# Kernel optimization log

Hardware: AMD Instinct MI355X
Metric: run time of the kernel (lower is better)

The kernel has to match this reference:

```python
import jax, jax.numpy as jnp
import numpy as np

N = 100_000          # num nodes
E = 1_600_000        # undirected edges (mean_degree = 2E/N = 32)
Q = 8                # num_groups
NUM_ITER = 5         # fixed BP iterations (max_num_iter)


def setup_inputs() -> dict:
    key = jax.random.key(0)
    k1, k2, k3, k4 = jax.random.split(key, 4)
    u = jax.random.randint(k1, (E,), 0, N, dtype=jnp.int32)
    v = jax.random.randint(k2, (E,), 0, N, dtype=jnp.int32)
    # directed messages: both orientations of every undirected edge
    src = jnp.concatenate([u, v])                 # [2E] message source i of i->j
    dst = jnp.concatenate([v, u])                 # [2E] message target j of i->j
    # rev[e] = index of the reverse message j->i for edge e = i->j
    rev = jnp.concatenate([jnp.arange(E, 2 * E, dtype=jnp.int32),
                           jnp.arange(E, dtype=jnp.int32)])
    psi0 = jax.random.uniform(k3, (N, Q), dtype=jnp.float32)
    msg0 = jax.random.uniform(k4, (2 * E, Q), dtype=jnp.float32)
    c = 2.0 * E / N  # mean degree
    beta = jnp.asarray(np.log(Q / np.sqrt(c - 1.0) + 1.0), dtype=jnp.float32)
    return dict(beta=beta, psi0=psi0, msg0=msg0, src=src, dst=dst, rev=rev,
                num_iter=NUM_ITER)


def reference(beta, psi0, msg0, src, dst, rev, num_iter):
    N_, Q_ = psi0.shape
    M = msg0.shape[0]
    mean_w = M / (N_ * N_)  # adjacency_matrix.mean() = 2E / N^2 (unweighted)
    psi = psi0 / psi0.sum(1, keepdims=True)   # normalized marginals [N,Q]
    msg = msg0 / msg0.sum(1, keepdims=True)   # normalized messages  [M,Q]
    h = (-beta * mean_w * psi).sum(0)         # external field        [Q]

    def step(carry, _):
        msg, psi, h = carry
        c = jnp.expm1(beta)                          # e^beta - 1
        # per-incoming-edge factor, in log space (scatter_mul -> segment_sum of logs)
        log_f = jnp.log1p(msg * c)                   # [M,Q]
        S = jax.ops.segment_sum(log_f, dst, num_segments=N_)  # [N,Q] prod over k->i
        # message i->j: exclude contribution of reverse edge j->i (cavity)
        logits = h + S[src] - log_f[rev]             # [M,Q]
        new_msg = jax.nn.softmax(logits, axis=-1)    # normalized per message
        diff = jnp.max(jnp.abs(new_msg - msg))
        # marginals from updated messages
        log_f2 = jnp.log1p(new_msg * c)
        S2 = jax.ops.segment_sum(log_f2, dst, num_segments=N_)
        new_psi = jax.nn.softmax(h + S2, axis=-1)    # [N,Q]
        new_h = (-beta * mean_w * new_psi).sum(0)    # [Q]
        return (new_msg, new_psi, new_h), diff

    (msg, psi, h), diffs = jax.lax.scan(step, (msg, psi, h), None, length=int(num_iter))
    return msg, psi, diffs[-1]
```

## Files before the change

### kernel.cpp

```cpp
#include <hip/hip_runtime.h>
#include <math.h>

#define Q 8
#define NUM_ITER 5
#define BLOCK 256
#define EBLK 1024
#define BLOCKA 512
#define NBN 1024
#define NBSHIFT 10
#define MAXBKT 128
#define W 4
#define QS 262144.0f
#define GRED 512

__device__ __forceinline__ void load8(const float* __restrict__ p, float v[Q]) {
    float4 a = ((const float4*)p)[0];
    float4 b = ((const float4*)p)[1];
    v[0]=a.x; v[1]=a.y; v[2]=a.z; v[3]=a.w;
    v[4]=b.x; v[5]=b.y; v[6]=b.z; v[7]=b.w;
}

__device__ __forceinline__ void store8(float* __restrict__ p, const float v[Q]) {
    ((float4*)p)[0] = make_float4(v[0],v[1],v[2],v[3]);
    ((float4*)p)[1] = make_float4(v[4],v[5],v[6],v[7]);
}

__device__ __forceinline__ void softmax8_fast(float l[Q]) {
    float mx = l[0];
    #pragma unroll
    for (int q=1;q<Q;q++) mx = fmaxf(mx, l[q]);
    float s = 0.f;
    #pragma unroll
    for (int q=0;q<Q;q++) { l[q] = __expf(l[q]-mx); s += l[q]; }
    float inv = 1.0f/s;
    #pragma unroll
    for (int q=0;q<Q;q++) l[q] *= inv;
}

__device__ __forceinline__ void pack18(const float lf[Q], int loc, uint4& a, unsigned& x) {
    unsigned v[Q];
    #pragma unroll
    for (int q=0;q<Q;q++) v[q] = (unsigned)__float2int_rn(lf[q]*QS);
    a.x = (v[0]&0xFFFFu) | ((v[1]&0xFFFFu)<<16);
    a.y = (v[2]&0xFFFFu) | ((v[3]&0xFFFFu)<<16);
    a.z = (v[4]&0xFFFFu) | ((v[5]&0xFFFFu)<<16);
    a.w = (v[6]&0xFFFFu) | ((v[7]&0xFFFFu)<<16);
    x = (v[0]>>16) | ((v[1]>>16)<<2) | ((v[2]>>16)<<4) | ((v[3]>>16)<<6)
      | ((v[4]>>16)<<8) | ((v[5]>>16)<<10) | ((v[6]>>16)<<12) | ((v[7]>>16)<<14)
      | ((unsigned)loc<<16);
}

__global__ void k_count(const int* __restrict__ src, const int* __restrict__ dst,
                        int* __restrict__ bcnt, int E, int nbkt) {
    __shared__ int c[4][MAXBKT];
    int wv = threadIdx.x >> 6;
    for (int t=threadIdx.x; t<4*MAXBKT; t+=BLOCK) ((int*)c)[t]=0;
    __syncthreads();
    for (int k = blockIdx.x*BLOCK + threadIdx.x; k < E; k += gridDim.x*BLOCK) {
        atomicAdd(&c[wv][dst[k]>>NBSHIFT], 1);
        atomicAdd(&c[wv][src[k]>>NBSHIFT], 1);
    }
    __syncthreads();
    for (int t=threadIdx.x; t<nbkt; t+=BLOCK) {
        int s = c[0][t]+c[1][t]+c[2][t]+c[3][t];
        if (s) atomicAdd(&bcnt[t], s);
    }
}

__global__ void k_scan(const int* __restrict__ bcnt, int* __restrict__ bucket_start,
                       int* __restrict__ cursor_g, int nbkt) {
    if (threadIdx.x==0 && blockIdx.x==0) {
        int run = 0;
        for (int b=0;b<nbkt;b++) { bucket_start[b]=run; cursor_g[b*16]=run; run += bcnt[b]; }
        bucket_start[nbkt] = run;
    }
}

__global__ void k_psi_init(const float* __restrict__ psi0,
                           const float* __restrict__ beta_p,
                           float mean_w, double* __restrict__ h0, int N) {
    int i = blockIdx.x*BLOCK + threadIdx.x;
    float c[Q];
    #pragma unroll
    for (int q=0;q<Q;q++) c[q]=0.f;
    if (i < N) {
        float p[Q]; load8(psi0 + (size_t)i*Q, p);
        float s = 0.f;
        #pragma unroll
        for (int q=0;q<Q;q++) s += p[q];
        float scale = -beta_p[0]*mean_w/s;
        #pragma unroll
        for (int q=0;q<Q;q++) c[q] = p[q]*scale;
    }
    __shared__ double sm[BLOCK/64][Q];
    #pragma unroll
    for (int q=0;q<Q;q++) {
        double x = (double)c[q];
        #pragma unroll
        for (int off=32;off;off>>=1) x += __shfl_down(x,off);
        if ((threadIdx.x&63)==0) sm[threadIdx.x>>6][q]=x;
    }
    __syncthreads();
    if (threadIdx.x < Q) {
        double x = sm[0][threadIdx.x]+sm[1][threadIdx.x]+sm[2][threadIdx.x]+sm[3][threadIdx.x];
        atomicAdd(h0+threadIdx.x, x);
    }
}

__global__ __launch_bounds__(EBLK) void k_init(const float* __restrict__ msg0,
                       const int* __restrict__ src, const int* __restrict__ dst,
                       const float* __restrict__ beta_p,
                       float* __restrict__ msg,
                       uint4* __restrict__ ebuf_q, unsigned* __restrict__ ebuf_x,
                       int* __restrict__ cursor_g, int E, int nbkt) {
    __shared__ int cnt[MAXBKT], excl[MAXBKT], base[MAXBKT];
    __shared__ int totsh;
    __shared__ uint4 staged[2*EBLK];
    __shared__ unsigned staged_x[2*EBLK];
    __shared__ int gpos[2*EBLK];
    int tid = threadIdx.x;
    for (int t=tid; t<MAXBKT; t+=EBLK) cnt[t]=0;
    __syncthreads();
    int k = blockIdx.x*EBLK + tid;
    bool act = (k < E);
    int b1=0,b2=0,o1=0,o2=0;
    uint4 p1, p2; unsigned x1, x2;
    if (act) {
        float cc = expm1f(beta_p[0]);
        int i = src[k], j = dst[k];
        float a[Q], b[Q];
        load8(msg0 + (size_t)k*Q, a);
        load8(msg0 + ((size_t)k+E)*Q, b);
        float sa=0.f, sb=0.f;
        #pragma unroll
        for (int q=0;q<Q;q++) { sa += a[q]; sb += b[q]; }
        float ia = 1.0f/sa, ib = 1.0f/sb;
        #pragma unroll
        for (int q=0;q<Q;q++) { a[q]*=ia; b[q]*=ib; }
        store8(msg + (size_t)k*Q, a);
        store8(msg + ((size_t)k+E)*Q, b);
        float lfa[Q], lfb[Q];
        #pragma unroll
        for (int q=0;q<Q;q++) {
            lfa[q] = __logf(fmaf(a[q], cc, 1.0f));
            lfb[q] = __logf(fmaf(b[q], cc, 1.0f));
        }
        b1 = j>>NBSHIFT; b2 = i>>NBSHIFT;
        o1 = atomicAdd(&cnt[b1], 1);
        o2 = atomicAdd(&cnt[b2], 1);
        pack18(lfa, j & (NBN-1), p1, x1);
        pack18(lfb, i & (NBN-1), p2, x2);
    }
    __syncthreads();
    if (tid < 64) {
        int a = cnt[2*tid], b = cnt[2*tid+1];
        int s = a+b;
        int incl = s;
        #pragma unroll
        for (int d=1; d<64; d<<=1) {
            int v = __shfl_up(incl, d);
            if (tid >= d) incl += v;
        }
        int exclp = incl - s;
        excl[2*tid]   = exclp;
        excl[2*tid+1] = exclp + a;
        if (tid==63) totsh = incl;
        base[2*tid]   = a ? atomicAdd(&cursor_g[(2*tid)*16], a) : 0;
        base[2*tid+1] = b ? atomicAdd(&cursor_g[(2*tid+1)*16], b) : 0;
    }
    __syncthreads();
    if (act) {
        int s1 = excl[b1]+o1; staged[s1]=p1; staged_x[s1]=x1; gpos[s1]=base[b1]+o1;
        int s2 = excl[b2]+o2; staged[s2]=p2; staged_x[s2]=x2; gpos[s2]=base[b2]+o2;
    }
    __syncthreads();
    int total = totsh;
    for (int s=tid; s<total; s+=EBLK) {
        int g = gpos[s];
        ebuf_q[g] = staged[s];
        ebuf_x[g] = staged_x[s];
    }
}

template<bool LAST>
__global__ __launch_bounds__(EBLK) void k_edge(const int* __restrict__ src,
                       const int* __restrict__ dst,
                       const float* __restrict__ beta_p,
                       const double* __restrict__ h, const float* __restrict__ Sf,
                       float* __restrict__ msg,
                       uint4* __restrict__ ebuf_q, unsigned* __restrict__ ebuf_x,
                       int* __restrict__ cursor_g,
                       float* __restrict__ diff_out,
                       int E, int nbkt) {
    __shared__ int cnt[MAXBKT], excl[MAXBKT], base[MAXBKT];
    __shared__ int totsh;
    __shared__ uint4 staged[2*EBLK];
    __shared__ unsigned staged_x[2*EBLK];
    __shared__ int gpos[2*EBLK];
    int tid = threadIdx.x;
    for (int t=tid; t<MAXBKT; t+=EBLK) cnt[t]=0;
    __syncthreads();
    int k = blockIdx.x*EBLK + tid;
    bool act = (k < E);
    float lmax = 0.f;
    int b1=0,b2=0,o1=0,o2=0;
    uint4 p1, p2; unsigned x1, x2;
    if (act) {
        float cc = expm1f(beta_p[0]);
        int i = src[k], j = dst[k];
        float m1[Q], m2[Q];
        load8(msg + (size_t)k*Q,       m1);
        load8(msg + ((size_t)k+E)*Q,   m2);
        float hv[Q];
        #pragma unroll
        for (int q=0;q<Q;q++) hv[q] = (float)h[q];
        float Si[Q], Sj[Q];
        load8(Sf + (size_t)i*Q, Si);
        load8(Sf + (size_t)j*Q, Sj);
        float l1[Q], l2[Q];
        #pragma unroll
        for (int q=0;q<Q;q++) {
            float lf1 = __logf(fmaf(m1[q], cc, 1.0f));
            float lf2 = __logf(fmaf(m2[q], cc, 1.0f));
            l1[q] = hv[q] + Si[q] - lf2;
            l2[q] = hv[q] + Sj[q] - lf1;
        }
        softmax8_fast(l1);
        softmax8_fast(l2);
        if (LAST) {
            #pragma unroll
            for (int q=0;q<Q;q++) {
                lmax = fmaxf(lmax, fabsf(l1[q]-m1[q]));
                lmax = fmaxf(lmax, fabsf(l2[q]-m2[q]));
            }
        }
        store8(msg + (size_t)k*Q,     l1);
        store8(msg + ((size_t)k+E)*Q, l2);
        float lf1n[Q], lf2n[Q];
        #pragma unroll
        for (int q=0;q<Q;q++) {
            lf1n[q] = __logf(fmaf(l1[q], cc, 1.0f));
            lf2n[q] = __logf(fmaf(l2[q], cc, 1.0f));
        }
        b1 = j>>NBSHIFT; b2 = i>>NBSHIFT;
        o1 = atomicAdd(&cnt[b1], 1);
        o2 = atomicAdd(&cnt[b2], 1);
        pack18(lf1n, j & (NBN-1), p1, x1);
        pack18(lf2n, i & (NBN-1), p2, x2);
    }
    __syncthreads();
    if (tid < 64) {
        int a = cnt[2*tid], b = cnt[2*tid+1];
        int s = a+b;
        int incl = s;
        #pragma unroll
        for (int d=1; d<64; d<<=1) {
            int v = __shfl_up(incl, d);
            if (tid >= d) incl += v;
        }
        int exclp = incl - s;
        excl[2*tid]   = exclp;
        excl[2*tid+1] = exclp + a;
        if (tid==63) totsh = incl;
        base[2*tid]   = a ? atomicAdd(&cursor_g[(2*tid)*16], a) : 0;
        base[2*tid+1] = b ? atomicAdd(&cursor_g[(2*tid+1)*16], b) : 0;
    }
    __syncthreads();
    if (act) {
        int s1 = excl[b1]+o1; staged[s1]=p1; staged_x[s1]=x1; gpos[s1]=base[b1]+o1;
        int s2 = excl[b2]+o2; staged[s2]=p2; staged_x[s2]=x2; gpos[s2]=base[b2]+o2;
    }
    __syncthreads();
    int total = totsh;
    for (int s=tid; s<total; s+=EBLK) {
        int g = gpos[s];
        ebuf_q[g] = staged[s];
        ebuf_x[g] = staged_x[s];
    }
    if (LAST) {
        float x = lmax;
        #pragma unroll
        for (int off=32;off;off>>=1) x = fmaxf(x, __shfl_down(x,off));
        __shared__ float smx[EBLK/64];
        if ((tid&63)==0) smx[tid>>6]=x;
        __syncthreads();
        if (tid==0) {
            float bmax = smx[0];
            #pragma unroll
            for (int t=1;t<EBLK/64;t++) bmax = fmaxf(bmax, smx[t]);
            atomicMax((unsigned int*)diff_out, __float_as_uint(bmax));
        }
    }
}

__global__ __launch_bounds__(BLOCKA) void k_accum(const uint4* __restrict__ ebuf_q,
                                                  const unsigned* __restrict__ ebuf_x,
                                                  const int* __restrict__ bucket_start,
                                                  unsigned long long* __restrict__ partials,
                                                  int* __restrict__ cursor_g) {
    __shared__ unsigned long long Sl[NBN*4];
    int wg = blockIdx.x;
    int b = wg / W, w = wg % W;
    for (int t=threadIdx.x*4; t<NBN*8; t+=BLOCKA*4) *(int4*)((int*)Sl+t) = make_int4(0,0,0,0);
    int lo = bucket_start[b], hi = bucket_start[b+1];
    if (w==0 && threadIdx.x==0) cursor_g[b*16] = lo;
    __syncthreads();
    int len = hi - lo;
    int l0 = lo + (int)(((long long)len * w) / W);
    int l1 = lo + (int)(((long long)len * (w+1)) / W);
    for (int s = l0 + threadIdx.x; s < l1; s += BLOCKA) {
        uint4 v = ebuf_q[s];
        unsigned x = ebuf_x[s];
        int loc = (int)(x >> 16);
        unsigned long long v0 = (v.x&0xFFFFu) | ((x&3u)<<16);
        unsigned long long v1 = (v.x>>16)     | (((x>>2)&3u)<<16);
        unsigned long long v2 = (v.y&0xFFFFu) | (((x>>4)&3u)<<16);
        unsigned long long v3 = (v.y>>16)     | (((x>>6)&3u)<<16);
        unsigned long long v4 = (v.z&0xFFFFu) | (((x>>8)&3u)<<16);
        unsigned long long v5 = (v.z>>16)     | (((x>>10)&3u)<<16);
        unsigned long long v6 = (v.w&0xFFFFu) | (((x>>12)&3u)<<16);
        unsigned long long v7 = (v.w>>16)     | (((x>>14)&3u)<<16);
        unsigned long long* p = Sl + loc*4;
        atomicAdd(p+0, v0 | (v1<<32));
        atomicAdd(p+1, v2 | (v3<<32));
        atomicAdd(p+2, v4 | (v5<<32));
        atomicAdd(p+3, v6 | (v7<<32));
    }
    __syncthreads();
    unsigned long long* outp = partials + (size_t)wg * (NBN*4);
    for (int t=threadIdx.x*4; t<NBN*8; t+=BLOCKA*4) *(int4*)((int*)outp+t) = *(const int4*)((const int*)Sl+t);
}

template<bool INIT, bool LAST>
__global__ __launch_bounds__(BLOCK) void k_reduce(const unsigned* __restrict__ pu,
                         const double* __restrict__ hcur,
                         const float* __restrict__ beta_p,
                         float mean_w, double* __restrict__ hnext,
                         float* __restrict__ Sf, float* __restrict__ psi_out, int N) {
    int q = threadIdx.x & 7;
    float hq = 0.f;
    if (!INIT) hq = (float)hcur[q];
    double pacc = 0.0;
    int total = N*8;
    int stride = BLOCK*GRED;
    for (int gid = blockIdx.x*BLOCK + threadIdx.x; gid < total; gid += stride) {
        int i = gid >> 3;
        int b = i >> NBSHIFT, loc = i & (NBN-1);
        unsigned s = 0;
        #pragma unroll
        for (int w=0; w<W; ++w) s += pu[(size_t)(b*W+w)*(NBN*8) + loc*8 + q];
        float Sv = (float)s * (1.0f/QS);
        Sf[gid] = Sv;
        if (!INIT) {
            float l = hq + Sv;
            float mx = l;
            #pragma unroll
            for (int m8=1;m8<8;m8<<=1) mx = fmaxf(mx, __shfl_xor(mx, m8));
            float ex = __expf(l - mx);
            float sum = ex;
            #pragma unroll
            for (int m8=1;m8<8;m8<<=1) sum += __shfl_xor(sum, m8);
            float p = ex / sum;
            if (LAST) psi_out[gid] = p;
            pacc += (double)p;
        }
    }
    if (!INIT) {
        double x = pacc;
        #pragma unroll
        for (int m8=8;m8<64;m8<<=1) x += __shfl_xor(x, m8);
        __shared__ double sm[BLOCK/64][Q];
        if ((threadIdx.x&63) < Q) sm[threadIdx.x>>6][threadIdx.x&7] = x;
        __syncthreads();
        if (threadIdx.x < Q) {
            double t = sm[0][threadIdx.x]+sm[1][threadIdx.x]+sm[2][threadIdx.x]+sm[3][threadIdx.x];
            double scale = -(double)beta_p[0]*(double)mean_w;
            atomicAdd(hnext+threadIdx.x, t*scale);
        }
    }
}

extern "C" void kernel_launch(void* const* d_in, const int* in_sizes, int n_in,
                              void* d_out, int out_size, void* d_ws, size_t ws_size,
                              hipStream_t stream) {
    const float* beta = (const float*)d_in[0];
    const float* psi0 = (const float*)d_in[1];
    const float* msg0 = (const float*)d_in[2];
    const int*   src  = (const int*)d_in[3];
    const int*   dst  = (const int*)d_in[4];

    int N = in_sizes[1] / Q;
    int M = in_sizes[2] / Q;
    int E = M / 2;
    int nbkt = (N + NBN - 1) / NBN;
    float mean_w = (float)((double)M / ((double)N * (double)N));

    float* out_msg  = (float*)d_out;
    float* out_psi  = out_msg + (size_t)M*Q;
    float* out_diff = out_psi + (size_t)N*Q;

    char* p = (char*)d_ws;
    double* hb[2];
    hb[0] = (double*)p;                      p += 2*Q*sizeof(double);
    hb[1] = hb[0] + Q;
    unsigned long long* partials = (unsigned long long*)p;  p += (size_t)nbkt*W*NBN*4*sizeof(unsigned long long);
    float* Sf = (float*)p;                   p += (size_t)N*Q*sizeof(float);
    uint4* ebuf_q = (uint4*)p;               p += (size_t)M*sizeof(uint4);
    unsigned* ebuf_x = (unsigned*)p;         p += (size_t)M*sizeof(unsigned);
    int* bcnt = (int*)p;                     p += MAXBKT*sizeof(int);
    int* bucket_start = (int*)p;             p += (MAXBKT+1)*sizeof(int);
    int* cursor_g = (int*)p;

    int geE   = (E + EBLK-1)/EBLK;
    int gn    = (N + BLOCK-1)/BLOCK;
    int gacc  = nbkt * W;

    hipMemsetAsync(hb[0], 0, Q*sizeof(double), stream);
    hipMemsetAsync(bcnt, 0, MAXBKT*sizeof(int), stream);

    k_count<<<256,BLOCK,0,stream>>>(src, dst, bcnt, E, nbkt);
    k_scan<<<1,64,0,stream>>>(bcnt, bucket_start, cursor_g, nbkt);
    k_init<<<geE,EBLK,0,stream>>>(msg0, src, dst, beta, out_msg, ebuf_q, ebuf_x,
                                  cursor_g, E, nbkt);
    k_psi_init<<<gn,BLOCK,0,stream>>>(psi0, beta, mean_w, hb[0], N);
    k_accum<<<gacc,BLOCKA,0,stream>>>(ebuf_q, ebuf_x, bucket_start, partials, cursor_g);
    k_reduce<true,false><<<GRED,BLOCK,0,stream>>>((const unsigned*)partials, hb[0], beta,
                                                  mean_w, hb[1], Sf, out_psi, N);

    int cur = 0;
    for (int t=0; t<NUM_ITER; ++t) {
        int nxt = cur^1;
        hipMemsetAsync(hb[nxt], 0, Q*sizeof(double), stream);
        if (t == NUM_ITER-1) {
            hipMemsetAsync(out_diff, 0, sizeof(float), stream);
            k_edge<true ><<<geE,EBLK,0,stream>>>(src,dst,beta,hb[cur],Sf,out_msg,
                                                 ebuf_q,ebuf_x,cursor_g,out_diff,E,nbkt);
            k_accum<<<gacc,BLOCKA,0,stream>>>(ebuf_q, ebuf_x, bucket_start, partials, cursor_g);
            k_reduce<false,true ><<<GRED,BLOCK,0,stream>>>((const unsigned*)partials, hb[cur], beta,
                                                           mean_w, hb[nxt], Sf, out_psi, N);
        } else {
            k_edge<false><<<geE,EBLK,0,stream>>>(src,dst,beta,hb[cur],Sf,out_msg,
                                                 ebuf_q,ebuf_x,cursor_g,out_diff,E,nbkt);
            k_accum<<<gacc,BLOCKA,0,stream>>>(ebuf_q, ebuf_x, bucket_start, partials, cursor_g);
            k_reduce<false,false><<<GRED,BLOCK,0,stream>>>((const unsigned*)partials, hb[cur], beta,
                                                           mean_w, hb[nxt], Sf, out_psi, N);
        }
        cur = nxt;
    }
}
```

Baseline: 668.1 us.

## Carry messages between iterations as packed quantized log-factors instead of fp32

Edge kernels now keep each message's log1p(msg*c) in a packed 18-bit fixed-point form (20 bytes per message) instead of storing the fp32 normalized message (32 bytes). This cuts per-iteration message read and write traffic and removes the per-iteration log computation on the old messages. Full fp32 messages are written only in the last iteration, and the convergence diff is rebuilt from the dequantized log-factors. The risk is accuracy: the messages fed into the next iteration and the diff now carry quantization error.

```diff
diff --git a/kernel.cpp b/kernel.cpp
--- a/kernel.cpp
+++ b/kernel.cpp
@@ -50,6 +50,17 @@
       | ((unsigned)loc<<16);
 }
 
+__device__ __forceinline__ void dq18(uint4 a, unsigned x, float lf[Q]) {
+    lf[0] = (float)((a.x & 0xFFFFu) | ((x     &3u)<<16)) * (1.0f/QS);
+    lf[1] = (float)((a.x >> 16)     | (((x>>2 )&3u)<<16)) * (1.0f/QS);
+    lf[2] = (float)((a.y & 0xFFFFu) | (((x>>4 )&3u)<<16)) * (1.0f/QS);
+    lf[3] = (float)((a.y >> 16)     | (((x>>6 )&3u)<<16)) * (1.0f/QS);
+    lf[4] = (float)((a.z & 0xFFFFu) | (((x>>8 )&3u)<<16)) * (1.0f/QS);
+    lf[5] = (float)((a.z >> 16)     | (((x>>10)&3u)<<16)) * (1.0f/QS);
+    lf[6] = (float)((a.w & 0xFFFFu) | (((x>>12)&3u)<<16)) * (1.0f/QS);
+    lf[7] = (float)((a.w >> 16)     | (((x>>14)&3u)<<16)) * (1.0f/QS);
+}
+
 __global__ void k_count(const int* __restrict__ src, const int* __restrict__ dst,
                         int* __restrict__ bcnt, int E, int nbkt) {
     __shared__ int c[4][MAXBKT];
@@ -110,7 +121,7 @@
 __global__ __launch_bounds__(EBLK) void k_init(const float* __restrict__ msg0,
                        const int* __restrict__ src, const int* __restrict__ dst,
                        const float* __restrict__ beta_p,
-                       float* __restrict__ msg,
+                       uint4* __restrict__ lfe_q, unsigned* __restrict__ lfe_x,
                        uint4* __restrict__ ebuf_q, unsigned* __restrict__ ebuf_x,
                        int* __restrict__ cursor_g, int E, int nbkt) {
     __shared__ int cnt[MAXBKT], excl[MAXBKT], base[MAXBKT];
@@ -137,8 +148,6 @@
         float ia = 1.0f/sa, ib = 1.0f/sb;
         #pragma unroll
         for (int q=0;q<Q;q++) { a[q]*=ia; b[q]*=ib; }
-        store8(msg + (size_t)k*Q, a);
-        store8(msg + ((size_t)k+E)*Q, b);
         float lfa[Q], lfb[Q];
         #pragma unroll
         for (int q=0;q<Q;q++) {
@@ -150,6 +159,8 @@
         o2 = atomicAdd(&cnt[b2], 1);
         pack18(lfa, j & (NBN-1), p1, x1);
         pack18(lfb, i & (NBN-1), p2, x2);
+        lfe_q[k]   = p1; lfe_x[k]   = x1;
+        lfe_q[k+E] = p2; lfe_x[k+E] = x2;
     }
     __syncthreads();
     if (tid < 64) {
@@ -187,7 +198,8 @@
                        const int* __restrict__ dst,
                        const float* __restrict__ beta_p,
                        const double* __restrict__ h, const float* __restrict__ Sf,
-                       float* __restrict__ msg,
+                       uint4* __restrict__ lfe_q, unsigned* __restrict__ lfe_x,
+                       float* __restrict__ out_msg,
                        uint4* __restrict__ ebuf_q, unsigned* __restrict__ ebuf_x,
                        int* __restrict__ cursor_g,
                        float* __restrict__ diff_out,
@@ -208,9 +220,9 @@
     if (act) {
         float cc = expm1f(beta_p[0]);
         int i = src[k], j = dst[k];
-        float m1[Q], m2[Q];
-        load8(msg + (size_t)k*Q,       m1);
-        load8(msg + ((size_t)k+E)*Q,   m2);
+        float lf1o[Q], lf2o[Q];
+        dq18(lfe_q[k],   lfe_x[k],   lf1o);
+        dq18(lfe_q[k+E], lfe_x[k+E], lf2o);
         float hv[Q];
         #pragma unroll
         for (int q=0;q<Q;q++) hv[q] = (float)h[q];
@@ -220,22 +232,23 @@
         float l1[Q], l2[Q];
         #pragma unroll
         for (int q=0;q<Q;q++) {
-            float lf1 = __logf(fmaf(m1[q], cc, 1.0f));
-            float lf2 = __logf(fmaf(m2[q], cc, 1.0f));
-            l1[q] = hv[q] + Si[q] - lf2;
-            l2[q] = hv[q] + Sj[q] - lf1;
+            l1[q] = hv[q] + Si[q] - lf2o[q];
+            l2[q] = hv[q] + Sj[q] - lf1o[q];
         }
         softmax8_fast(l1);
         softmax8_fast(l2);
         if (LAST) {
+            float icc = 1.0f/cc;
             #pragma unroll
             for (int q=0;q<Q;q++) {
-                lmax = fmaxf(lmax, fabsf(l1[q]-m1[q]));
-                lmax = fmaxf(lmax, fabsf(l2[q]-m2[q]));
+                float m1o = (__expf(lf1o[q]) - 1.0f) * icc;
+                float m2o = (__expf(lf2o[q]) - 1.0f) * icc;
+                lmax = fmaxf(lmax, fabsf(l1[q]-m1o));
+                lmax = fmaxf(lmax, fabsf(l2[q]-m2o));
             }
-        }
-        store8(msg + (size_t)k*Q,     l1);
-        store8(msg + ((size_t)k+E)*Q, l2);
+            store8(out_msg + (size_t)k*Q,     l1);
+            store8(out_msg + ((size_t)k+E)*Q, l2);
+        }
         float lf1n[Q], lf2n[Q];
         #pragma unroll
         for (int q=0;q<Q;q++) {
@@ -247,6 +260,8 @@
         o2 = atomicAdd(&cnt[b2], 1);
         pack18(lf1n, j & (NBN-1), p1, x1);
         pack18(lf2n, i & (NBN-1), p2, x2);
+        lfe_q[k]   = p1; lfe_x[k]   = x1;
+        lfe_q[k+E] = p2; lfe_x[k+E] = x2;
     }
     __syncthreads();
     if (tid < 64) {
@@ -405,7 +420,9 @@
     hb[1] = hb[0] + Q;
     unsigned long long* partials = (unsigned long long*)p;  p += (size_t)nbkt*W*NBN*4*sizeof(unsigned long long);
     float* Sf = (float*)p;                   p += (size_t)N*Q*sizeof(float);
+    uint4* lfe_q = (uint4*)p;                p += (size_t)M*sizeof(uint4);
     uint4* ebuf_q = (uint4*)p;               p += (size_t)M*sizeof(uint4);
+    unsigned* lfe_x = (unsigned*)p;          p += (size_t)M*sizeof(unsigned);
     unsigned* ebuf_x = (unsigned*)p;         p += (size_t)M*sizeof(unsigned);
     int* bcnt = (int*)p;                     p += MAXBKT*sizeof(int);
     int* bucket_start = (int*)p;             p += (MAXBKT+1)*sizeof(int);
@@ -420,7 +437,7 @@
 
     k_count<<<256,BLOCK,0,stream>>>(src, dst, bcnt, E, nbkt);
     k_scan<<<1,64,0,stream>>>(bcnt, bucket_start, cursor_g, nbkt);
-    k_init<<<geE,EBLK,0,stream>>>(msg0, src, dst, beta, out_msg, ebuf_q, ebuf_x,
+    k_init<<<geE,EBLK,0,stream>>>(msg0, src, dst, beta, lfe_q, lfe_x, ebuf_q, ebuf_x,
                                   cursor_g, E, nbkt);
     k_psi_init<<<gn,BLOCK,0,stream>>>(psi0, beta, mean_w, hb[0], N);
     k_accum<<<gacc,BLOCKA,0,stream>>>(ebuf_q, ebuf_x, bucket_start, partials, cursor_g);
@@ -433,13 +450,13 @@
         hipMemsetAsync(hb[nxt], 0, Q*sizeof(double), stream);
         if (t == NUM_ITER-1) {
             hipMemsetAsync(out_diff, 0, sizeof(float), stream);
-            k_edge<true ><<<geE,EBLK,0,stream>>>(src,dst,beta,hb[cur],Sf,out_msg,
+            k_edge<true ><<<geE,EBLK,0,stream>>>(src,dst,beta,hb[cur],Sf,lfe_q,lfe_x,out_msg,
                                                  ebuf_q,ebuf_x,cursor_g,out_diff,E,nbkt);
             k_accum<<<gacc,BLOCKA,0,stream>>>(ebuf_q, ebuf_x, bucket_start, partials, cursor_g);
             k_reduce<false,true ><<<GRED,BLOCK,0,stream>>>((const unsigned*)partials, hb[cur], beta,
                                                            mean_w, hb[nxt], Sf, out_psi, N);
         } else {
-            k_edge<false><<<geE,EBLK,0,stream>>>(src,dst,beta,hb[cur],Sf,out_msg,
+            k_edge<false><<<geE,EBLK,0,stream>>>(src,dst,beta,hb[cur],Sf,lfe_q,lfe_x,out_msg,
                                                  ebuf_q,ebuf_x,cursor_g,out_diff,E,nbkt);
             k_accum<<<gacc,BLOCKA,0,stream>>>(ebuf_q, ebuf_x, bucket_start, partials, cursor_g);
             k_reduce<false,false><<<GRED,BLOCK,0,stream>>>((const unsigned*)partials, hb[cur], beta,
```

Result: faster. 619.8 us (-7.2%).
